# Performance work log

Measured on AMD Instinct MI355X. Metric: run time of the kernel, lower is better.

Reference implementation:

```python
import jax, jax.numpy as jnp
import numpy as np

SIZES = [4096, 12288, 20480, 20480, 8192]  # atoms of degree 0..4 (atoms sorted by degree)
N_ATOMS = sum(SIZES)
BATCH = 1024
N_TASKS, N_CLASSES = 12, 2
BN_EPS = 1e-3  # keras BatchNormalization default epsilon


def setup_inputs() -> dict:
    key = jax.random.key(0)
    ks = jax.random.split(key, 20)
    inp = {}
    inp["atom_features"] = jax.random.normal(ks[0], (N_ATOMS, 75), jnp.float32)
    starts = np.concatenate([[0], np.cumsum(SIZES)[:-1]])
    inp["degree_slice"] = jnp.asarray(np.stack([starts, np.array(SIZES)], 1), jnp.int32)
    inp["membership"] = jax.random.randint(ks[1], (N_ATOMS,), 0, BATCH, jnp.int32)
    inp["n_samples"] = BATCH
    for d in range(1, 5):
        inp[f"deg_adj_{d}"] = jax.random.randint(ks[1 + d], (SIZES[d], d), 0, N_ATOMS, jnp.int32)

    def w(k, shape, s=0.05):
        return s * jax.random.normal(k, shape, jnp.float32)

    # GraphConv weights: order [relW_deg1, selfW_deg1, ..., relW_deg4, selfW_deg4, selfW_deg0]
    inp["gc1_W"] = w(ks[6], (9, 75, 256)); inp["gc1_b"] = w(ks[7], (9, 256))
    inp["gc2_W"] = w(ks[8], (9, 256, 256)); inp["gc2_b"] = w(ks[9], (9, 256))

    def bn_params(k, c):  # rows: gamma, beta, moving_mean, moving_var
        g = 1.0 + 0.1 * jax.random.normal(k, (c,), jnp.float32)
        b = 0.1 * jax.random.normal(jax.random.fold_in(k, 1), (c,), jnp.float32)
        return jnp.stack([g, b, jnp.zeros((c,), jnp.float32), jnp.ones((c,), jnp.float32)])

    inp["bn1"] = bn_params(ks[10], 256)
    inp["bn2"] = bn_params(ks[11], 256)
    inp["bn3"] = bn_params(ks[12], 512)
    inp["dense_W"] = w(ks[13], (256, 512)); inp["dense_b"] = w(ks[14], (512,))
    inp["head_W"] = w(ks[15], (2 * 512, N_TASKS * N_CLASSES)); inp["head_b"] = w(ks[16], (N_TASKS * N_CLASSES,))
    return inp


def _graph_conv(x, adjs, W, b):
    # degree-0 atoms: self transform only (last weight matrix)
    pieces = [x[: SIZES[0]] @ W[8] + b[8]]
    off = SIZES[0]
    for d in range(1, 5):
        nd = SIZES[d]
        self_atoms = x[off: off + nd]
        rel = jnp.take(x, adjs[d - 1], axis=0).sum(axis=1)  # [nd, F] neighbor sum
        out = rel @ W[2 * (d - 1)] + b[2 * (d - 1)] + self_atoms @ W[2 * d - 1] + b[2 * d - 1]
        pieces.append(out)
        off += nd
    return jax.nn.relu(jnp.concatenate(pieces, axis=0))


def _graph_pool(x, adjs):
    pieces = [x[: SIZES[0]]]  # degree-0: passthrough
    off = SIZES[0]
    for d in range(1, 5):
        nd = SIZES[d]
        self_atoms = x[off: off + nd]
        neigh = jnp.take(x, adjs[d - 1], axis=0)  # [nd, d, F]
        pieces.append(jnp.maximum(self_atoms, neigh.max(axis=1)))
        off += nd
    return jnp.concatenate(pieces, axis=0)


def _bn(x, p):  # inference batchnorm with moving stats
    g, b, m, v = p
    return g * (x - m) * jax.lax.rsqrt(v + BN_EPS) + b


def reference(atom_features, degree_slice, membership, n_samples,
              deg_adj_1, deg_adj_2, deg_adj_3, deg_adj_4,
              gc1_W, gc1_b, gc2_W, gc2_b, bn1, bn2, bn3,
              dense_W, dense_b, head_W, head_b):
    adjs = (deg_adj_1, deg_adj_2, deg_adj_3, deg_adj_4)
    x = atom_features
    for W, b, bn in ((gc1_W, gc1_b, bn1), (gc2_W, gc2_b, bn2)):
        x = _bn(_graph_conv(x, adjs, W, b), bn)
        x = _graph_pool(x, adjs)
    h = _bn(jax.nn.relu(x @ dense_W + dense_b), bn3)  # [N_ATOMS, 512]
    # GraphGather: per-molecule sum and max, tanh activation
    seg_sum = jax.ops.segment_sum(h, membership, num_segments=BATCH)
    seg_max = jax.ops.segment_max(h, membership, num_segments=BATCH)
    fp = jnp.tanh(jnp.concatenate([seg_sum, seg_max], axis=1))  # neural fingerprint [BATCH, 1024]
    logits = (fp @ head_W + head_b).reshape(BATCH, N_TASKS, N_CLASSES)[: int(n_samples)]  # trim
    return jax.nn.softmax(logits, axis=-1), logits, fp
```

## Files before the change

kernel.cpp:

```cpp
#include <hip/hip_runtime.h>
#include <hip/hip_bf16.h>
#include <math.h>

#define NA 65536
#define MAXSEG 160

typedef _Float16 half8 __attribute__((ext_vector_type(8)));
typedef _Float16 h4    __attribute__((ext_vector_type(4)));
typedef float float4v  __attribute__((ext_vector_type(4)));


__device__ __forceinline__ void atom_seg(int atom, int& d, int& loc,
                                         const int* a1, const int* a2,
                                         const int* a3, const int* a4,
                                         const int*& adj) {
    if (atom < 4096)       { d = 0; loc = 0; adj = nullptr; }
    else if (atom < 16384) { d = 1; adj = a1; loc = atom - 4096; }
    else if (atom < 36864) { d = 2; adj = a2; loc = atom - 16384; }
    else if (atom < 57344) { d = 3; adj = a3; loc = atom - 36864; }
    else                   { d = 4; adj = a4; loc = atom - 57344; }
}

__global__ void zero_count_kernel(int* __restrict__ count) {
    int i = blockIdx.x * 256 + threadIdx.x;
    if (i < 1024) count[i] = 0;
}

__global__ void bucket_kernel(const int* __restrict__ mem, int* __restrict__ count,
                              int* __restrict__ list) {
    int i = blockIdx.x * 256 + threadIdx.x;
    int seg = mem[i];
    int pos = atomicAdd(&count[seg], 1);
    if (pos < MAXSEG) list[seg * MAXSEG + pos] = i;
}

__global__ void cvt_w1_kernel(const float* __restrict__ gc1W, const float* __restrict__ gc1b,
                              _Float16* __restrict__ Wc1, float* __restrict__ bias1) {
    int idx = blockIdx.x * 256 + threadIdx.x;
    if (idx < 204800) {
        int k = idx % 160, n = (idx / 160) & 255, seg = idx / (160 * 256);
        float v = 0.f;
        if (k < 75) { int w = (seg == 0) ? 8 : (2 * seg - 1); v = gc1W[(w * 75 + k) * 256 + n]; }
        else if (k < 150 && seg > 0) { int w = 2 * (seg - 1); v = gc1W[(w * 75 + (k - 75)) * 256 + n]; }
        Wc1[(size_t)(seg * 256 + n) * 160 + k] = (_Float16)v;
    }
    if (idx < 1280) {
        int n = idx & 255, seg = idx >> 8;
        bias1[idx] = (seg == 0) ? gc1b[8 * 256 + n]
                                : gc1b[(2 * seg - 1) * 256 + n] + gc1b[2 * (seg - 1) * 256 + n];
    }
}

__global__ void cvt_w2_kernel(const float* __restrict__ gc2W, const float* __restrict__ gc2b,
                              _Float16* __restrict__ Wc2, float* __restrict__ bias2) {
    int idx = blockIdx.x * 256 + threadIdx.x;
    if (idx < 655360) {
        int k = idx & 511, n = (idx >> 9) & 255, seg = idx >> 17;
        float v = 0.f;
        if (k < 256) { int w = (seg == 0) ? 8 : (2 * seg - 1); v = gc2W[(w * 256 + k) * 256 + n]; }
        else if (seg > 0) { int w = 2 * (seg - 1); v = gc2W[(w * 256 + (k - 256)) * 256 + n]; }
        Wc2[(size_t)(seg * 256 + n) * 512 + k] = (_Float16)v;
    }
    if (idx < 1280) {
        int n = idx & 255, seg = idx >> 8;
        bias2[idx] = (seg == 0) ? gc2b[8 * 256 + n]
                                : gc2b[(2 * seg - 1) * 256 + n] + gc2b[2 * (seg - 1) * 256 + n];
    }
}

__global__ void cvt_wd_kernel(const float* __restrict__ dW, _Float16* __restrict__ dWt) {
    int idx = blockIdx.x * 256 + threadIdx.x;
    int n = idx >> 8, k = idx & 255;
    dWt[(size_t)n * 256 + k] = (_Float16)dW[(size_t)k * 512 + n];
}

__global__ void cvt_hw_kernel(const float* __restrict__ hW, float* __restrict__ hWt) {
    int idx = blockIdx.x * 256 + threadIdx.x;
    int o = idx / 1024, k = idx & 1023;
    hWt[idx] = hW[k * 24 + o];
}

__global__ __launch_bounds__(256) void gather1_kernel(
    const float* __restrict__ af,
    const int* __restrict__ a1, const int* __restrict__ a2,
    const int* __restrict__ a3, const int* __restrict__ a4,
    _Float16* __restrict__ X1) {
    int atom = blockIdx.x * 4 + (threadIdx.x >> 6);
    int lane = threadIdx.x & 63;
    int d, loc; const int* adj;
    atom_seg(atom, d, loc, a1, a2, a3, a4, adj);
    int nb[4];
    for (int j = 0; j < d; j++) nb[j] = adj[(size_t)loc * d + j];
    for (int k = lane; k < 75; k += 64) {
        X1[(size_t)atom * 160 + k] = (_Float16)af[(size_t)atom * 75 + k];
        float s = 0.f;
        for (int j = 0; j < d; j++) s += af[(size_t)nb[j] * 75 + k];
        X1[(size_t)atom * 160 + 75 + k] = (_Float16)s;
    }
    if (lane < 10) X1[(size_t)atom * 160 + 150 + lane] = (_Float16)0.f;
}

__global__ __launch_bounds__(256) void gather2n_kernel(
    const _Float16* __restrict__ p,
    const int* __restrict__ a1, const int* __restrict__ a2,
    const int* __restrict__ a3, const int* __restrict__ a4,
    _Float16* __restrict__ Xn) {
    int atom = blockIdx.x * 4 + (threadIdx.x >> 6);
    int lane = threadIdx.x & 63;
    int d, loc; const int* adj;
    atom_seg(atom, d, loc, a1, a2, a3, a4, adj);
    int nb[4];
    for (int j = 0; j < d; j++) nb[j] = adj[(size_t)loc * d + j];
    float s0 = 0.f, s1 = 0.f, s2 = 0.f, s3 = 0.f;
    for (int j = 0; j < d; j++) {
        h4 v = *(const h4*)(p + (size_t)nb[j] * 256 + lane * 4);
        s0 += (float)v[0]; s1 += (float)v[1]; s2 += (float)v[2]; s3 += (float)v[3];
    }
    h4 o; o[0] = (_Float16)s0; o[1] = (_Float16)s1; o[2] = (_Float16)s2; o[3] = (_Float16)s3;
    *(h4*)(Xn + (size_t)atom * 256 + lane * 4) = o;
}

template<int K, int N, int BK, int SPLIT>
__global__ __launch_bounds__(256) void gemm_kernel(
    const _Float16* __restrict__ X, const _Float16* __restrict__ Xn,
    const _Float16* __restrict__ Wt,
    const float* __restrict__ bias, const float* __restrict__ bnp,
    int wstride, int bstride, _Float16* __restrict__ out) {
    constexpr int NC8 = BK / 8;
    __shared__ _Float16 As[128 * BK];
    __shared__ _Float16 Bs[128 * BK];
    constexpr int nb = N / 128;
    int bid = blockIdx.x;
    int m0 = (bid / nb) * 128, n0 = (bid % nb) * 128;
    int t = m0 >> 7;
    int seg = (t < 32) ? 0 : (t < 128) ? 1 : (t < 288) ? 2 : (t < 448) ? 3 : 4;
    const _Float16* Wb = Wt + (size_t)seg * wstride;
    const float* bia = bias + seg * bstride;
    int tid = threadIdx.x, lane = tid & 63, wave = tid >> 6;
    int wm = (wave >> 1) * 64, wn = (wave & 1) * 64;
    int lrow = lane & 15, lq = lane >> 4;
    float4v acc[4][4] = {};
    for (int kc = 0; kc < K / BK; kc++) {
        #pragma unroll
        for (int p = tid; p < 128 * NC8; p += 256) {
            int row = p / NC8, c8 = p % NC8;
            int cs = c8 ^ (row & (NC8 - 1));
            const _Float16* srcA;
            if (!SPLIT) {
                srcA = X + (size_t)(m0 + row) * K + kc * BK + c8 * 8;
            } else {
                int kcol = kc * BK + c8 * 8;
                srcA = (kcol < 256) ? X  + (size_t)(m0 + row) * 256 + kcol
                                    : Xn + (size_t)(m0 + row) * 256 + (kcol - 256);
            }
            *(uint4*)(As + row * BK + cs * 8) = *(const uint4*)srcA;
            *(uint4*)(Bs + row * BK + cs * 8) =
                *(const uint4*)(Wb + (size_t)(n0 + row) * K + kc * BK + c8 * 8);
        }
        __syncthreads();
        #pragma unroll
        for (int kl = 0; kl < BK / 32; kl++) {
            half8 af[4], bf[4];
            #pragma unroll
            for (int i = 0; i < 4; i++) {
                int ra = wm + i * 16 + lrow;
                int ca = (kl * 4 + lq) ^ (ra & (NC8 - 1));
                af[i] = *(const half8*)(As + ra * BK + ca * 8);
                int rb = wn + i * 16 + lrow;
                int cb = (kl * 4 + lq) ^ (rb & (NC8 - 1));
                bf[i] = *(const half8*)(Bs + rb * BK + cb * 8);
            }
            #pragma unroll
            for (int mi = 0; mi < 4; mi++)
                #pragma unroll
                for (int ni = 0; ni < 4; ni++)
                    acc[mi][ni] = __builtin_amdgcn_mfma_f32_16x16x32_f16(af[mi], bf[ni], acc[mi][ni], 0, 0, 0);
        }
        __syncthreads();
    }
    #pragma unroll
    for (int ni = 0; ni < 4; ni++) {
        int col = n0 + wn + ni * 16 + lrow;
        float bv = bia[col], g = bnp[col], be = bnp[N + col];
        float mn = bnp[2 * N + col], vr = bnp[3 * N + col];
        float sc = g * rsqrtf(vr + 1e-3f);
        #pragma unroll
        for (int mi = 0; mi < 4; mi++) {
            int rbase = m0 + wm + mi * 16 + lq * 4;
            #pragma unroll
            for (int r = 0; r < 4; r++) {
                float v = acc[mi][ni][r] + bv;
                v = fmaxf(v, 0.f);
                v = sc * (v - mn) + be;
                out[(size_t)(rbase + r) * N + col] = (_Float16)v;
            }
        }
    }
}

__global__ __launch_bounds__(256) void pool_f16_kernel(
    const _Float16* __restrict__ x,
    const int* __restrict__ a1, const int* __restrict__ a2,
    const int* __restrict__ a3, const int* __restrict__ a4,
    _Float16* __restrict__ out) {
    int atom = blockIdx.x * 4 + (threadIdx.x >> 6);
    int lane = threadIdx.x & 63;
    int d, loc; const int* adj;
    atom_seg(atom, d, loc, a1, a2, a3, a4, adj);
    h4 m = *(const h4*)(x + (size_t)atom * 256 + lane * 4);
    float m0 = (float)m[0], m1 = (float)m[1], m2 = (float)m[2], m3 = (float)m[3];
    for (int j = 0; j < d; j++) {
        int nb = adj[(size_t)loc * d + j];
        h4 v = *(const h4*)(x + (size_t)nb * 256 + lane * 4);
        m0 = fmaxf(m0, (float)v[0]); m1 = fmaxf(m1, (float)v[1]);
        m2 = fmaxf(m2, (float)v[2]); m3 = fmaxf(m3, (float)v[3]);
    }
    h4 o; o[0] = (_Float16)m0; o[1] = (_Float16)m1; o[2] = (_Float16)m2; o[3] = (_Float16)m3;
    *(h4*)(out + (size_t)atom * 256 + lane * 4) = o;
}

__global__ __launch_bounds__(512) void seg_reduce_kernel(
    const _Float16* __restrict__ h, const int* __restrict__ count,
    const int* __restrict__ list, float* __restrict__ fp) {
    int seg = blockIdx.x, c = threadIdx.x;
    int n = count[seg]; if (n > MAXSEG) n = MAXSEG;
    float sum = 0.f, mx = -INFINITY;
    for (int a = 0; a < n; a++) {
        int row = list[seg * MAXSEG + a];
        float v = (float)h[(size_t)row * 512 + c];
        sum += v; mx = fmaxf(mx, v);
    }
    fp[(size_t)seg * 1024 + c] = tanhf(sum);
    fp[(size_t)seg * 1024 + 512 + c] = tanhf(mx);
}

__global__ __launch_bounds__(256) void head_kernel(
    const float* __restrict__ fp, const float* __restrict__ hWt,
    const float* __restrict__ hb, float* __restrict__ logits,
    float* __restrict__ probs) {
    __shared__ float fps[1024];
    __shared__ float red[32];
    int s = blockIdx.x;
    for (int i = threadIdx.x; i < 1024; i += 256) fps[i] = fp[(size_t)s * 1024 + i];
    __syncthreads();
    int t = threadIdx.x;
    int o = t >> 3, kp = t & 7;
    float acc = 0.f;
    if (o < 24) {
        const float* w = hWt + (size_t)o * 1024 + kp * 128;
        const float* f = fps + kp * 128;
        #pragma unroll 8
        for (int i = 0; i < 128; i++) acc = fmaf(f[i], w[i], acc);
    }
    acc += __shfl_down(acc, 4, 64);
    acc += __shfl_down(acc, 2, 64);
    acc += __shfl_down(acc, 1, 64);
    if (o < 24 && kp == 0) red[o] = acc + hb[o];
    __syncthreads();
    if (t < 24) {
        float a = red[t];
        float an = red[t ^ 1];
        logits[(size_t)s * 24 + t] = a;
        probs[(size_t)s * 24 + t] = 1.f / (1.f + expf(an - a));
    }
}

extern "C" void kernel_launch(void* const* d_in, const int* in_sizes, int n_in,
                              void* d_out, int out_size, void* d_ws, size_t ws_size,
                              hipStream_t stream) {
    const float* af         = (const float*)d_in[0];
    const int*   membership = (const int*)d_in[2];
    const int*   a1 = (const int*)d_in[4];
    const int*   a2 = (const int*)d_in[5];
    const int*   a3 = (const int*)d_in[6];
    const int*   a4 = (const int*)d_in[7];
    const float* gc1W = (const float*)d_in[8];
    const float* gc1b = (const float*)d_in[9];
    const float* gc2W = (const float*)d_in[10];
    const float* gc2b = (const float*)d_in[11];
    const float* bn1  = (const float*)d_in[12];
    const float* bn2  = (const float*)d_in[13];
    const float* bn3  = (const float*)d_in[14];
    const float* dW   = (const float*)d_in[15];
    const float* db   = (const float*)d_in[16];
    const float* hW   = (const float*)d_in[17];
    const float* hb   = (const float*)d_in[18];

    float* out    = (float*)d_out;
    float* probs  = out;
    float* logits = out + 24576;
    float* fp     = out + 49152;

    _Float16* Wc1  = (_Float16*)d_ws;
    _Float16* Wc2  = Wc1 + 204800;
    _Float16* dWt  = Wc2 + 655360;
    float* bias1   = (float*)(dWt + 131072);
    float* bias2   = bias1 + 1280;
    float* hWt     = bias2 + 1280;
    int* count     = (int*)(hWt + 24576);
    int* list      = count + 1024;
    _Float16* bufBig = (_Float16*)(list + 163840);
    _Float16* bufY   = bufBig + (size_t)NA * 512;
    _Float16* bufP   = bufY + (size_t)NA * 256;
    _Float16* X1 = bufBig;
    _Float16* Xn = bufBig + (size_t)NA * 256;
    _Float16* h  = bufBig;

    zero_count_kernel<<<4, 256, 0, stream>>>(count);
    bucket_kernel<<<256, 256, 0, stream>>>(membership, count, list);
    cvt_w1_kernel<<<800, 256, 0, stream>>>(gc1W, gc1b, Wc1, bias1);
    cvt_w2_kernel<<<2560, 256, 0, stream>>>(gc2W, gc2b, Wc2, bias2);
    cvt_wd_kernel<<<512, 256, 0, stream>>>(dW, dWt);
    cvt_hw_kernel<<<96, 256, 0, stream>>>(hW, hWt);

    gather1_kernel<<<16384, 256, 0, stream>>>(af, a1, a2, a3, a4, X1);
    gemm_kernel<160, 256, 32, 0><<<1024, 256, 0, stream>>>(X1, nullptr, Wc1, bias1, bn1,
                                                           256 * 160, 256, bufY);
    pool_f16_kernel<<<16384, 256, 0, stream>>>(bufY, a1, a2, a3, a4, bufP);
    gather2n_kernel<<<16384, 256, 0, stream>>>(bufP, a1, a2, a3, a4, Xn);
    gemm_kernel<512, 256, 64, 1><<<1024, 256, 0, stream>>>(bufP, Xn, Wc2, bias2, bn2,
                                                           256 * 512, 256, bufY);
    pool_f16_kernel<<<16384, 256, 0, stream>>>(bufY, a1, a2, a3, a4, bufP);
    gemm_kernel<256, 512, 64, 0><<<2048, 256, 0, stream>>>(bufP, nullptr, dWt, db, bn3,
                                                           0, 0, h);
    seg_reduce_kernel<<<1024, 512, 0, stream>>>(h, count, list, fp);
    head_kernel<<<1024, 256, 0, stream>>>(fp, hWt, hb, logits, probs);
}
```

Before: 368.7 us.

## Store GEMM outputs as packed 16-byte rows with permuted channels, swizzle block order

```diff
diff --git a/kernel.cpp b/kernel.cpp
--- a/kernel.cpp
+++ b/kernel.cpp
@@ -9,6 +9,10 @@
 typedef _Float16 h4    __attribute__((ext_vector_type(4)));
 typedef float float4v  __attribute__((ext_vector_type(4)));
 
+
+__device__ __forceinline__ int unperm128(int p) {
+    return (p & ~127) + (((p & 127) & 7) << 4) + ((p & 127) >> 3);
+}
 
 __device__ __forceinline__ void atom_seg(int atom, int& d, int& loc,
                                          const int* a1, const int* a2,
@@ -57,8 +61,15 @@
     if (idx < 655360) {
         int k = idx & 511, n = (idx >> 9) & 255, seg = idx >> 17;
         float v = 0.f;
-        if (k < 256) { int w = (seg == 0) ? 8 : (2 * seg - 1); v = gc2W[(w * 256 + k) * 256 + n]; }
-        else if (seg > 0) { int w = 2 * (seg - 1); v = gc2W[(w * 256 + (k - 256)) * 256 + n]; }
+        if (k < 256) {
+            int w = (seg == 0) ? 8 : (2 * seg - 1);
+            int chan = unperm128(k);
+            v = gc2W[(w * 256 + chan) * 256 + n];
+        } else if (seg > 0) {
+            int w = 2 * (seg - 1);
+            int chan = unperm128(k - 256);
+            v = gc2W[(w * 256 + chan) * 256 + n];
+        }
         Wc2[(size_t)(seg * 256 + n) * 512 + k] = (_Float16)v;
     }
     if (idx < 1280) {
@@ -71,7 +82,7 @@
 __global__ void cvt_wd_kernel(const float* __restrict__ dW, _Float16* __restrict__ dWt) {
     int idx = blockIdx.x * 256 + threadIdx.x;
     int n = idx >> 8, k = idx & 255;
-    dWt[(size_t)n * 256 + k] = (_Float16)dW[(size_t)k * 512 + n];
+    dWt[(size_t)n * 256 + k] = (_Float16)dW[(size_t)unperm128(k) * 512 + n];
 }
 
 __global__ void cvt_hw_kernel(const float* __restrict__ hW, float* __restrict__ hWt) {
@@ -130,16 +141,17 @@
     __shared__ _Float16 As[128 * BK];
     __shared__ _Float16 Bs[128 * BK];
     constexpr int nb = N / 128;
-    int bid = blockIdx.x;
+    int G = gridDim.x;
+    int bid = (blockIdx.x & 7) * (G >> 3) + (blockIdx.x >> 3);
     int m0 = (bid / nb) * 128, n0 = (bid % nb) * 128;
     int t = m0 >> 7;
     int seg = (t < 32) ? 0 : (t < 128) ? 1 : (t < 288) ? 2 : (t < 448) ? 3 : 4;
     const _Float16* Wb = Wt + (size_t)seg * wstride;
     const float* bia = bias + seg * bstride;
     int tid = threadIdx.x, lane = tid & 63, wave = tid >> 6;
-    int wm = (wave >> 1) * 64, wn = (wave & 1) * 64;
+    int wm = wave * 32;
     int lrow = lane & 15, lq = lane >> 4;
-    float4v acc[4][4] = {};
+    float4v acc[2][8] = {};
     for (int kc = 0; kc < K / BK; kc++) {
         #pragma unroll
         for (int p = tid; p < 128 * NC8; p += 256) {
@@ -160,40 +172,50 @@
         __syncthreads();
         #pragma unroll
         for (int kl = 0; kl < BK / 32; kl++) {
-            half8 af[4], bf[4];
+            half8 af[2], bf[8];
             #pragma unroll
-            for (int i = 0; i < 4; i++) {
+            for (int i = 0; i < 2; i++) {
                 int ra = wm + i * 16 + lrow;
                 int ca = (kl * 4 + lq) ^ (ra & (NC8 - 1));
                 af[i] = *(const half8*)(As + ra * BK + ca * 8);
-                int rb = wn + i * 16 + lrow;
-                int cb = (kl * 4 + lq) ^ (rb & (NC8 - 1));
-                bf[i] = *(const half8*)(Bs + rb * BK + cb * 8);
             }
             #pragma unroll
-            for (int mi = 0; mi < 4; mi++)
+            for (int j = 0; j < 8; j++) {
+                int rb = j * 16 + lrow;
+                int cb = (kl * 4 + lq) ^ (rb & (NC8 - 1));
+                bf[j] = *(const half8*)(Bs + rb * BK + cb * 8);
+            }
+            #pragma unroll
+            for (int mi = 0; mi < 2; mi++)
                 #pragma unroll
-                for (int ni = 0; ni < 4; ni++)
+                for (int ni = 0; ni < 8; ni++)
                     acc[mi][ni] = __builtin_amdgcn_mfma_f32_16x16x32_f16(af[mi], bf[ni], acc[mi][ni], 0, 0, 0);
         }
         __syncthreads();
     }
+    float bv[8], sc[8], mn[8], be[8];
     #pragma unroll
-    for (int ni = 0; ni < 4; ni++) {
-        int col = n0 + wn + ni * 16 + lrow;
-        float bv = bia[col], g = bnp[col], be = bnp[N + col];
-        float mn = bnp[2 * N + col], vr = bnp[3 * N + col];
-        float sc = g * rsqrtf(vr + 1e-3f);
+    for (int ni = 0; ni < 8; ni++) {
+        int c = n0 + ni * 16 + lrow;
+        bv[ni] = bia[c];
+        float g = bnp[c], vr = bnp[3 * N + c];
+        mn[ni] = bnp[2 * N + c]; be[ni] = bnp[N + c];
+        sc[ni] = g * rsqrtf(vr + 1e-3f);
+    }
+    #pragma unroll
+    for (int mi = 0; mi < 2; mi++) {
         #pragma unroll
-        for (int mi = 0; mi < 4; mi++) {
-            int rbase = m0 + wm + mi * 16 + lq * 4;
+        for (int r = 0; r < 4; r++) {
+            half8 pack;
             #pragma unroll
-            for (int r = 0; r < 4; r++) {
-                float v = acc[mi][ni][r] + bv;
+            for (int ni = 0; ni < 8; ni++) {
+                float v = acc[mi][ni][r] + bv[ni];
                 v = fmaxf(v, 0.f);
-                v = sc * (v - mn) + be;
-                out[(size_t)(rbase + r) * N + col] = (_Float16)v;
+                v = sc[ni] * (v - mn[ni]) + be[ni];
+                pack[ni] = (_Float16)v;
             }
+            int row = m0 + wm + mi * 16 + lq * 4 + r;
+            *(half8*)(out + (size_t)row * N + n0 + lrow * 8) = pack;
         }
     }
 }
@@ -223,6 +245,7 @@
     const _Float16* __restrict__ h, const int* __restrict__ count,
     const int* __restrict__ list, float* __restrict__ fp) {
     int seg = blockIdx.x, c = threadIdx.x;
+    int chan = unperm128(c);
     int n = count[seg]; if (n > MAXSEG) n = MAXSEG;
     float sum = 0.f, mx = -INFINITY;
     for (int a = 0; a < n; a++) {
@@ -230,8 +253,8 @@
         float v = (float)h[(size_t)row * 512 + c];
         sum += v; mx = fmaxf(mx, v);
     }
-    fp[(size_t)seg * 1024 + c] = tanhf(sum);
-    fp[(size_t)seg * 1024 + 512 + c] = tanhf(mx);
+    fp[(size_t)seg * 1024 + chan] = tanhf(sum);
+    fp[(size_t)seg * 1024 + 512 + chan] = tanhf(mx);
 }
 
 __global__ __launch_bounds__(256) void head_kernel(
```

Result: no change. 364.2 us (-1.2%).
